# Kernel tuning notes

Hardware: AMD Instinct MI355X
Metric: run time of the kernel (lower is better)

The kernel has to match this reference:

```python
import jax, jax.numpy as jnp
import numpy as np

DIM = 128
BATCH = 262144
N_PAIRS = DIM * (DIM - 1) // 2  # 8128

# Static pair ordering exactly as in the torch module: (i, j) for i in range(dim) for j in range(i+1, dim)
_p = np.array([(i, j) for i in range(DIM) for j in range(i + 1, DIM)], dtype=np.int32)
I_IDX = jnp.asarray(_p[:, 0])
J_IDX = jnp.asarray(_p[:, 1])


def setup_inputs() -> dict:
    key = jax.random.key(0)
    k1, k2 = jax.random.split(key)
    x = jax.random.normal(k1, (BATCH, DIM), dtype=jnp.float32)
    angles = jax.random.normal(k2, (N_PAIRS,), dtype=jnp.float32) * 0.01
    bias = jnp.zeros((DIM,), dtype=jnp.float32)
    return {"x": x, "angles": angles, "bias": bias}


def _rotation_matrix(angles):
    # The layer is linear: applying the ordered Givens sweep to every row of x
    # equals x @ W where W is the sweep applied to eye(dim) (cf. weight_matrix()).
    # Building W via a scan over the 8128 rotations is the efficient faithful form.
    cos, sin = jnp.cos(angles), jnp.sin(angles)

    def step(W, vals):
        i, j, c, s = vals
        wi = W[:, i]  # [dim]
        wj = W[:, j]
        # out[:, [i,j]] @ [[c, -s], [s, c]]  ->  new_i = wi*c + wj*s ; new_j = wj*c - wi*s
        W = W.at[:, i].set(wi * c + wj * s)
        W = W.at[:, j].set(wj * c - wi * s)
        return W, None

    W0 = jnp.eye(DIM, dtype=angles.dtype)
    W, _ = jax.lax.scan(step, W0, (I_IDX, J_IDX, cos, sin))
    return W


def reference(x, angles, bias):
    W = _rotation_matrix(angles)  # [dim, dim] orthogonal
    return x @ W + bias
```

## Files before the change

### kernel.cpp

```cpp
#include <hip/hip_runtime.h>

typedef float  floatx4  __attribute__((ext_vector_type(4)));
typedef short  bf16x8   __attribute__((ext_vector_type(8)));
typedef float  facc4    __attribute__((ext_vector_type(4)));

__device__ __forceinline__ unsigned short f2bf(float f) {
  unsigned u = __builtin_bit_cast(unsigned, f);
  u = u + 0x7fffu + ((u >> 16) & 1u);
  return (unsigned short)(u >> 16);
}

__global__ void k_sincos(const float* __restrict__ ang, float* __restrict__ cs) {
  int i = blockIdx.x * 256 + threadIdx.x;
  if (i < 8128) {
    float s, c;
    sincosf(ang[i], &s, &c);
    cs[2 * i]     = c;
    cs[2 * i + 1] = s;
  }
}

template <int I0, int I1>
__device__ void gen_chunk(const float* __restrict__ cs, float* __restrict__ out, int row) {
  float w[128];
#pragma unroll
  for (int k = 0; k < 128; ++k) w[k] = (k == row) ? 1.0f : 0.0f;
#pragma unroll
  for (int i = I0; i < I1; ++i) {
    float wi = w[i];
#pragma unroll
    for (int j = i + 1; j < 128; ++j) {
      const int p = i * 127 - (i * (i - 1)) / 2 + (j - i - 1);
      const float c = cs[2 * p];
      const float s = cs[2 * p + 1];
      const float wj = w[j];
      const float nwi = fmaf(wj, s, wi * c);
      w[j] = fmaf(wj, c, -(wi * s));
      wi = nwi;
    }
    w[i] = wi;
  }
  floatx4* o = (floatx4*)(out + row * 128);
#pragma unroll
  for (int k = 0; k < 32; ++k) {
    floatx4 v;
    v[0] = w[4 * k]; v[1] = w[4 * k + 1]; v[2] = w[4 * k + 2]; v[3] = w[4 * k + 3];
    o[k] = v;
  }
}

__global__ __launch_bounds__(128) void k_chunks(const float* __restrict__ cs,
                                                float* __restrict__ out) {
  const int row = threadIdx.x;
  switch (blockIdx.x) {
    case 0:  gen_chunk<0,   8>(cs, out + 0 * 16384, row); break;
    case 1:  gen_chunk<8,  17>(cs, out + 1 * 16384, row); break;
    case 2:  gen_chunk<17, 27>(cs, out + 2 * 16384, row); break;
    case 3:  gen_chunk<27, 37>(cs, out + 3 * 16384, row); break;
    case 4:  gen_chunk<37, 49>(cs, out + 4 * 16384, row); break;
    case 5:  gen_chunk<49, 64>(cs, out + 5 * 16384, row); break;
    case 6:  gen_chunk<64, 82>(cs, out + 6 * 16384, row); break;
    default: gen_chunk<82, 127>(cs, out + 7 * 16384, row); break;
  }
}

__global__ __launch_bounds__(128) void k_combine(const float* __restrict__ chunks,
                                                 unsigned short* __restrict__ wt) {
  __shared__ float sv[128];
  const int r = blockIdx.x;
  const int t = threadIdx.x;
  float v = chunks[r * 128 + t];
#pragma unroll
  for (int m = 1; m < 8; ++m) {
    __syncthreads();
    sv[t] = v;
    __syncthreads();
    const float* Cm = chunks + m * 16384;
    float acc = 0.0f;
#pragma unroll
    for (int k = 0; k < 128; ++k) acc = fmaf(sv[k], Cm[k * 128 + t], acc);
    v = acc;
  }
  wt[t * 136 + r] = f2bf(v);
}

__global__ __launch_bounds__(256) void k_gemm(const float* __restrict__ x,
                                              const unsigned short* __restrict__ wt,
                                              const float* __restrict__ bias,
                                              float* __restrict__ y) {
  __shared__ unsigned short sW[128 * 136];
  __shared__ float sB[128];
  const int tid = threadIdx.x;
  {
    const floatx4* src = (const floatx4*)wt;
    floatx4* dst = (floatx4*)sW;
#pragma unroll
    for (int i2 = 0; i2 < 9; ++i2) {
      int idx = tid + i2 * 256;
      if (idx < 2176) dst[idx] = src[idx];
    }
    if (tid < 128) sB[tid] = bias[tid];
  }
  __syncthreads();

  const int wave = tid >> 6, lane = tid & 63;
  const int m16 = lane & 15, h = lane >> 4;

  for (int it = 0; it < 4; ++it) {
    const int base_row = blockIdx.x * 256 + (wave * 4 + it) * 16;
    const float* xr = x + (size_t)(base_row + m16) * 128;
    floatx4 a[8];
#pragma unroll
    for (int c = 0; c < 4; ++c) {
      a[2 * c]     = *(const floatx4*)(xr + c * 32 + h * 8);
      a[2 * c + 1] = *(const floatx4*)(xr + c * 32 + h * 8 + 4);
    }
    facc4 acc[8];
#pragma unroll
    for (int t = 0; t < 8; ++t) {
#pragma unroll
      for (int rr = 0; rr < 4; ++rr) acc[t][rr] = 0.0f;
    }
#pragma unroll
    for (int c = 0; c < 4; ++c) {
      bf16x8 af;
#pragma unroll
      for (int q = 0; q < 8; ++q) {
        const float f = (q < 4) ? a[2 * c][q] : a[2 * c + 1][q - 4];
        af[q] = (short)f2bf(f);
      }
#pragma unroll
      for (int t = 0; t < 8; ++t) {
        const bf16x8 bfr = *(const bf16x8*)(&sW[(t * 16 + m16) * 136 + c * 32 + h * 8]);
        acc[t] = __builtin_amdgcn_mfma_f32_16x16x32_bf16(af, bfr, acc[t], 0, 0, 0);
      }
    }
#pragma unroll
    for (int t = 0; t < 8; ++t) {
      const float b = sB[t * 16 + m16];
#pragma unroll
      for (int rr = 0; rr < 4; ++rr) {
        const int row = base_row + h * 4 + rr;
        y[(size_t)row * 128 + t * 16 + m16] = acc[t][rr] + b;
      }
    }
  }
}

extern "C" void kernel_launch(void* const* d_in, const int* in_sizes, int n_in,
                              void* d_out, int out_size, void* d_ws, size_t ws_size,
                              hipStream_t stream) {
  const float* x    = (const float*)d_in[0];
  const float* ang  = (const float*)d_in[1];
  const float* bias = (const float*)d_in[2];
  float* y = (float*)d_out;

  char* ws = (char*)d_ws;
  float* cs               = (float*)ws;
  float* chunks           = (float*)(ws + 65536);
  unsigned short* wt      = (unsigned short*)(ws + 65536 + 524288);

  k_sincos <<<32,   256, 0, stream>>>(ang, cs);
  k_chunks <<<8,    128, 0, stream>>>(cs, chunks);
  k_combine<<<128,  128, 0, stream>>>(chunks, wt);
  k_gemm   <<<1024, 256, 0, stream>>>(x, wt, bias, y);
}
```

Before: 310.6 us.

## Fuse sincos into chunk generation and vectorize GEMM stores via swapped MFMA operands

```diff
diff --git a/kernel.cpp b/kernel.cpp
--- a/kernel.cpp
+++ b/kernel.cpp
@@ -10,37 +10,38 @@
   return (unsigned short)(u >> 16);
 }
 
-__global__ void k_sincos(const float* __restrict__ ang, float* __restrict__ cs) {
-  int i = blockIdx.x * 256 + threadIdx.x;
-  if (i < 8128) {
+template <int I0, int I1>
+__device__ void gen_chunk(const float* __restrict__ ang, float* __restrict__ out,
+                          float* lcs, int tid) {
+  constexpr int P0 = I0 * 127 - I0 * (I0 - 1) / 2;
+  constexpr int P1 = I1 * 127 - I1 * (I1 - 1) / 2;
+  constexpr int NROT = P1 - P0;
+  for (int idx = tid; idx < NROT; idx += 256) {
     float s, c;
-    sincosf(ang[i], &s, &c);
-    cs[2 * i]     = c;
-    cs[2 * i + 1] = s;
+    sincosf(ang[P0 + idx], &s, &c);
+    lcs[2 * idx] = c;
+    lcs[2 * idx + 1] = s;
   }
-}
-
-template <int I0, int I1>
-__device__ void gen_chunk(const float* __restrict__ cs, float* __restrict__ out, int row) {
+  __syncthreads();
+  if (tid >= 128) return;
   float w[128];
 #pragma unroll
-  for (int k = 0; k < 128; ++k) w[k] = (k == row) ? 1.0f : 0.0f;
+  for (int k = 0; k < 128; ++k) w[k] = (k == tid) ? 1.0f : 0.0f;
 #pragma unroll
   for (int i = I0; i < I1; ++i) {
     float wi = w[i];
 #pragma unroll
     for (int j = i + 1; j < 128; ++j) {
-      const int p = i * 127 - (i * (i - 1)) / 2 + (j - i - 1);
-      const float c = cs[2 * p];
-      const float s = cs[2 * p + 1];
+      const int p = (i * 127 - (i * (i - 1)) / 2 + (j - i - 1)) - P0;
+      const float2 cs2 = *(const float2*)(&lcs[2 * p]);
+      const float c = cs2.x, s = cs2.y;
       const float wj = w[j];
-      const float nwi = fmaf(wj, s, wi * c);
       w[j] = fmaf(wj, c, -(wi * s));
-      wi = nwi;
+      wi   = fmaf(wj, s, wi * c);
     }
     w[i] = wi;
   }
-  floatx4* o = (floatx4*)(out + row * 128);
+  floatx4* o = (floatx4*)(out + (size_t)tid * 128);
 #pragma unroll
   for (int k = 0; k < 32; ++k) {
     floatx4 v;
@@ -49,18 +50,19 @@
   }
 }
 
-__global__ __launch_bounds__(128) void k_chunks(const float* __restrict__ cs,
-                                                float* __restrict__ out) {
-  const int row = threadIdx.x;
+__global__ __launch_bounds__(256) void k_wgen(const float* __restrict__ ang,
+                                              float* __restrict__ out) {
+  __shared__ float lcs[2144];
+  const int tid = threadIdx.x;
   switch (blockIdx.x) {
-    case 0:  gen_chunk<0,   8>(cs, out + 0 * 16384, row); break;
-    case 1:  gen_chunk<8,  17>(cs, out + 1 * 16384, row); break;
-    case 2:  gen_chunk<17, 27>(cs, out + 2 * 16384, row); break;
-    case 3:  gen_chunk<27, 37>(cs, out + 3 * 16384, row); break;
-    case 4:  gen_chunk<37, 49>(cs, out + 4 * 16384, row); break;
-    case 5:  gen_chunk<49, 64>(cs, out + 5 * 16384, row); break;
-    case 6:  gen_chunk<64, 82>(cs, out + 6 * 16384, row); break;
-    default: gen_chunk<82, 127>(cs, out + 7 * 16384, row); break;
+    case 0:  gen_chunk<0,   8>(ang, out + 0 * 16384, lcs, tid); break;
+    case 1:  gen_chunk<8,  17>(ang, out + 1 * 16384, lcs, tid); break;
+    case 2:  gen_chunk<17, 27>(ang, out + 2 * 16384, lcs, tid); break;
+    case 3:  gen_chunk<27, 37>(ang, out + 3 * 16384, lcs, tid); break;
+    case 4:  gen_chunk<37, 49>(ang, out + 4 * 16384, lcs, tid); break;
+    case 5:  gen_chunk<49, 64>(ang, out + 5 * 16384, lcs, tid); break;
+    case 6:  gen_chunk<64, 82>(ang, out + 6 * 16384, lcs, tid); break;
+    default: gen_chunk<82, 127>(ang, out + 7 * 16384, lcs, tid); break;
   }
 }
 
@@ -70,16 +72,20 @@
   const int r = blockIdx.x;
   const int t = threadIdx.x;
   float v = chunks[r * 128 + t];
-#pragma unroll
   for (int m = 1; m < 8; ++m) {
     __syncthreads();
     sv[t] = v;
     __syncthreads();
-    const float* Cm = chunks + m * 16384;
-    float acc = 0.0f;
+    const float* Cm = chunks + m * 16384 + t;
+    float a0 = 0.f, a1 = 0.f, a2 = 0.f, a3 = 0.f;
 #pragma unroll
-    for (int k = 0; k < 128; ++k) acc = fmaf(sv[k], Cm[k * 128 + t], acc);
-    v = acc;
+    for (int k = 0; k < 128; k += 4) {
+      a0 = fmaf(sv[k],     Cm[(k)     * 128], a0);
+      a1 = fmaf(sv[k + 1], Cm[(k + 1) * 128], a1);
+      a2 = fmaf(sv[k + 2], Cm[(k + 2) * 128], a2);
+      a3 = fmaf(sv[k + 3], Cm[(k + 3) * 128], a3);
+    }
+    v = (a0 + a1) + (a2 + a3);
   }
   wt[t * 136 + r] = f2bf(v);
 }
@@ -106,43 +112,51 @@
   const int wave = tid >> 6, lane = tid & 63;
   const int m16 = lane & 15, h = lane >> 4;
 
+  const size_t row0 = (size_t)blockIdx.x * 256 + wave * 64 + m16;
+  const float* xr0 = x + row0 * 128;
+  float* yr0 = y + row0 * 128;
+
+  floatx4 a[8];
+#pragma unroll
+  for (int c = 0; c < 4; ++c) {
+    a[2 * c]     = *(const floatx4*)(xr0 + c * 32 + h * 8);
+    a[2 * c + 1] = *(const floatx4*)(xr0 + c * 32 + h * 8 + 4);
+  }
+
+#pragma unroll
   for (int it = 0; it < 4; ++it) {
-    const int base_row = blockIdx.x * 256 + (wave * 4 + it) * 16;
-    const float* xr = x + (size_t)(base_row + m16) * 128;
-    floatx4 a[8];
+    bf16x8 af[4];
 #pragma unroll
     for (int c = 0; c < 4; ++c) {
-      a[2 * c]     = *(const floatx4*)(xr + c * 32 + h * 8);
-      a[2 * c + 1] = *(const floatx4*)(xr + c * 32 + h * 8 + 4);
+#pragma unroll
+      for (int q = 0; q < 8; ++q) {
+        const float f = (q < 4) ? a[2 * c][q] : a[2 * c + 1][q - 4];
+        af[c][q] = (short)f2bf(f);
+      }
+    }
+    if (it < 3) {
+      const float* xr = xr0 + (size_t)(it + 1) * 16 * 128;
+#pragma unroll
+      for (int c = 0; c < 4; ++c) {
+        a[2 * c]     = *(const floatx4*)(xr + c * 32 + h * 8);
+        a[2 * c + 1] = *(const floatx4*)(xr + c * 32 + h * 8 + 4);
+      }
     }
     facc4 acc[8];
 #pragma unroll
-    for (int t = 0; t < 8; ++t) {
-#pragma unroll
-      for (int rr = 0; rr < 4; ++rr) acc[t][rr] = 0.0f;
-    }
+    for (int t = 0; t < 8; ++t) acc[t] = *(const facc4*)(sB + t * 16 + h * 4);
 #pragma unroll
     for (int c = 0; c < 4; ++c) {
-      bf16x8 af;
-#pragma unroll
-      for (int q = 0; q < 8; ++q) {
-        const float f = (q < 4) ? a[2 * c][q] : a[2 * c + 1][q - 4];
-        af[q] = (short)f2bf(f);
-      }
 #pragma unroll
       for (int t = 0; t < 8; ++t) {
-        const bf16x8 bfr = *(const bf16x8*)(&sW[(t * 16 + m16) * 136 + c * 32 + h * 8]);
-        acc[t] = __builtin_amdgcn_mfma_f32_16x16x32_bf16(af, bfr, acc[t], 0, 0, 0);
+        const bf16x8 bw = *(const bf16x8*)(&sW[(t * 16 + m16) * 136 + c * 32 + h * 8]);
+        acc[t] = __builtin_amdgcn_mfma_f32_16x16x32_bf16(bw, af[c], acc[t], 0, 0, 0);
       }
     }
+    float* yr = yr0 + (size_t)it * 16 * 128;
 #pragma unroll
     for (int t = 0; t < 8; ++t) {
-      const float b = sB[t * 16 + m16];
-#pragma unroll
-      for (int rr = 0; rr < 4; ++rr) {
-        const int row = base_row + h * 4 + rr;
-        y[(size_t)row * 128 + t * 16 + m16] = acc[t][rr] + b;
-      }
+      *(floatx4*)(yr + t * 16 + h * 4) = acc[t];
     }
   }
 }
@@ -156,12 +170,10 @@
   float* y = (float*)d_out;
 
   char* ws = (char*)d_ws;
-  float* cs               = (float*)ws;
-  float* chunks           = (float*)(ws + 65536);
-  unsigned short* wt      = (unsigned short*)(ws + 65536 + 524288);
+  float* chunks      = (float*)ws;
+  unsigned short* wt = (unsigned short*)(ws + 524288);
 
-  k_sincos <<<32,   256, 0, stream>>>(ang, cs);
-  k_chunks <<<8,    128, 0, stream>>>(cs, chunks);
+  k_wgen   <<<8,    256, 0, stream>>>(ang, chunks);
   k_combine<<<128,  128, 0, stream>>>(chunks, wt);
   k_gemm   <<<1024, 256, 0, stream>>>(x, wt, bias, y);
 }
```

Result: faster. 288.3 us (-7.2%).
